# Optimization experiments

Measured on AMD Instinct MI355X. Metric: run time of the kernel, lower is better.

The kernel has to match this reference:

```python
import jax, jax.numpy as jnp
import numpy as np

N_EXPERTS = 8
D_MODEL = 1024
D_FF = 4096
BATCH = 4
SEQ = 4096


def setup_inputs() -> dict:
    key = jax.random.key(0)
    k1, k2, k3, k4 = jax.random.split(key, 4)
    hidden_states = jax.random.normal(k1, (BATCH, SEQ, D_MODEL), dtype=jnp.float32)
    expert_indices = jax.random.randint(k2, (BATCH, SEQ), 0, N_EXPERTS, dtype=jnp.int64)
    # Expert MLP params, scaled like standard init
    W1 = jax.random.normal(k3, (N_EXPERTS, D_MODEL, D_FF), dtype=jnp.float32) / np.sqrt(D_MODEL)
    b1 = jnp.zeros((N_EXPERTS, D_FF), dtype=jnp.float32)
    W2 = jax.random.normal(k4, (N_EXPERTS, D_FF, D_MODEL), dtype=jnp.float32) / np.sqrt(D_FF)
    b2 = jnp.zeros((N_EXPERTS, D_MODEL), dtype=jnp.float32)
    return {"hidden_states": hidden_states, "expert_indices": expert_indices,
            "W1": W1, "b1": b1, "W2": W2, "b2": b2}


def reference(hidden_states, expert_indices, W1, b1, W2, b2):
    B, S, D = hidden_states.shape
    flat = hidden_states.reshape(B * S, D)          # [T, D]
    idx = expert_indices.reshape(-1)                 # [T]
    out = jnp.zeros_like(flat)
    # Fixed small loop over experts (structurally distinct weights).
    # jit-friendly: each expert runs over all tokens, output masked per token.
    for e in range(W1.shape[0]):
        h = jax.nn.gelu(flat @ W1[e] + b1[e])        # [T, F]
        y = h @ W2[e] + b2[e]                        # [T, D]
        out = out + jnp.where((idx == e)[:, None], y, jnp.float32(0.0))
    return out.reshape(B, S, D)
```

## Files before the change

### kernel.cpp

```cpp
#include <hip/hip_runtime.h>

#define T_TOK 16384
#define DMODEL 1024
#define DFF 4096
#define NEXP 8
#define BM 128
#define BN 128
#define BK 32
#define LDA 40
#define LDB 40
#define TPAD (T_TOK + NEXP * BM)

typedef __bf16 bf16x8 __attribute__((ext_vector_type(8)));
typedef float f32x4 __attribute__((ext_vector_type(4)));

#define GLOAD16(gp, lp) __builtin_amdgcn_global_load_lds( \
    (const __attribute__((address_space(1))) void*)(gp), \
    (__attribute__((address_space(3))) void*)(lp), 16, 0, 0)

__device__ __forceinline__ float gelu_f(float x) {
  float u = 0.7978845608028654f * (x + 0.044715f * x * x * x);
  float e = __expf(2.0f * u);
  float th = 1.0f - 2.0f / (e + 1.0f);
  return 0.5f * x * (1.0f + th);
}

__global__ void k_init(int* counts, int* cursors, int* bucket, int n) {
  int i = blockIdx.x * blockDim.x + threadIdx.x;
  if (i < n) bucket[i] = -1;
  if (i < NEXP) { counts[i] = 0; cursors[i] = 0; }
}

__global__ void k_hist(const int* __restrict__ idx, int* counts) {
  int t = blockIdx.x * blockDim.x + threadIdx.x;
  if (t < T_TOK) atomicAdd(&counts[idx[t]], 1);
}

__global__ void k_scan(const int* __restrict__ counts, int* po) {
  if (threadIdx.x == 0 && blockIdx.x == 0) {
    int acc = 0;
    for (int e = 0; e < NEXP; e++) {
      po[e] = acc;
      acc += ((counts[e] + BM - 1) / BM) * BM;
    }
    po[NEXP] = acc;
  }
}

__global__ void k_scatter(const int* __restrict__ idx, const int* __restrict__ po,
                          int* cursors, int* bucket) {
  int t = blockIdx.x * blockDim.x + threadIdx.x;
  if (t < T_TOK) {
    int e = idx[t];
    int p = atomicAdd(&cursors[e], 1);
    bucket[po[e] + p] = t;
  }
}

__global__ __launch_bounds__(256) void k_gather(
    const float* __restrict__ X, const int* __restrict__ bucket,
    __bf16* __restrict__ Xg)
{
  const int r = blockIdx.x;
  const int t = bucket[r];
  const int c = threadIdx.x * 4;
  float4 v = {0.f, 0.f, 0.f, 0.f};
  if (t >= 0) v = *(const float4*)&X[(size_t)t * DMODEL + c];
  union { __bf16 h[4]; uint2 u; } cv;
  cv.h[0] = (__bf16)v.x; cv.h[1] = (__bf16)v.y;
  cv.h[2] = (__bf16)v.z; cv.h[3] = (__bf16)v.w;
  *(uint2*)&Xg[(size_t)r * DMODEL + c] = cv.u;
}

__global__ __launch_bounds__(256) void k_transpose(
    const float* __restrict__ W, __bf16* __restrict__ Wt, int K, int N)
{
  __shared__ float tile[64][65];
  const size_t msz = (size_t)K * N;
  const float* __restrict__ src = W + (size_t)blockIdx.z * msz;
  __bf16* __restrict__ dst = Wt + (size_t)blockIdx.z * msz;
  const int n0 = blockIdx.x * 64, k0 = blockIdx.y * 64;
  const int tc = threadIdx.x & 15, tr = threadIdx.x >> 4;
#pragma unroll
  for (int i = 0; i < 4; i++) {
    float4 v = *(const float4*)&src[(size_t)(k0 + tr + i * 16) * N + n0 + tc * 4];
    tile[tr + i * 16][tc * 4 + 0] = v.x;
    tile[tr + i * 16][tc * 4 + 1] = v.y;
    tile[tr + i * 16][tc * 4 + 2] = v.z;
    tile[tr + i * 16][tc * 4 + 3] = v.w;
  }
  __syncthreads();
#pragma unroll
  for (int i = 0; i < 4; i++) {
    const int n = tr + i * 16;
    union { __bf16 h[4]; uint2 u; } cv;
    cv.h[0] = (__bf16)tile[tc * 4 + 0][n];
    cv.h[1] = (__bf16)tile[tc * 4 + 1][n];
    cv.h[2] = (__bf16)tile[tc * 4 + 2][n];
    cv.h[3] = (__bf16)tile[tc * 4 + 3][n];
    *(uint2*)&dst[(size_t)(n0 + n) * K + k0 + tc * 4] = cv.u;
  }
}

__global__ __launch_bounds__(256, 2) void k_gemm1b(
    const __bf16* __restrict__ Ag, const __bf16* __restrict__ Wt,
    const float* __restrict__ b1, const int* __restrict__ po,
    __bf16* __restrict__ H)
{
  __shared__ __align__(16) __bf16 As[BM * BK];
  __shared__ __align__(16) __bf16 Bs[BN * BK];
  const int tid = threadIdx.x;
  const int row0 = (int)blockIdx.x * BM;
  if (row0 >= po[NEXP]) return;
  const int nb0 = (int)blockIdx.y * BN;

  int e = 0;
#pragma unroll
  for (int k = 1; k < NEXP; k++) e = (row0 >= po[k]) ? k : e;
  const __bf16* __restrict__ B = Wt + (size_t)e * DFF * DMODEL;

  f32x4 acc[4][4];
#pragma unroll
  for (int i = 0; i < 4; i++)
#pragma unroll
    for (int j = 0; j < 4; j++) acc[i][j] = (f32x4)0.0f;

  const int wave = tid >> 6;
  const int lane = tid & 63;
  const int wm = (wave & 1) * 64;
  const int wn = (wave >> 1) * 64;
  const int lm = lane & 15;
  const int lq = lane >> 4;

  const int sr = wave * 32 + (lane >> 2);
  const int skq = lane & 3;
  const __bf16* Aptr = Ag + (size_t)(row0 + sr) * DMODEL + skq * 8;
  const __bf16* Bptr = B + (size_t)(nb0 + sr) * DMODEL + skq * 8;
  __bf16* Al = &As[wave * 1024];
  __bf16* Bl = &Bs[wave * 1024];

  for (int k0 = 0; k0 < DMODEL; k0 += BK) {
    GLOAD16(Aptr + k0, Al);
    GLOAD16(Aptr + k0 + 16 * DMODEL, Al + 512);
    GLOAD16(Bptr + k0, Bl);
    GLOAD16(Bptr + k0 + 16 * DMODEL, Bl + 512);
    __syncthreads();

    bf16x8 af[4], bfr[4];
#pragma unroll
    for (int i = 0; i < 4; i++)
      af[i] = *(const bf16x8*)&As[(wm + i * 16 + lm) * BK + lq * 8];
#pragma unroll
    for (int j = 0; j < 4; j++)
      bfr[j] = *(const bf16x8*)&Bs[(wn + j * 16 + lm) * BK + lq * 8];
#pragma unroll
    for (int i = 0; i < 4; i++)
#pragma unroll
      for (int j = 0; j < 4; j++)
        acc[i][j] = __builtin_amdgcn_mfma_f32_16x16x32_bf16(af[i], bfr[j], acc[i][j], 0, 0, 0);
    __syncthreads();
  }

  const float* __restrict__ b1e = b1 + e * DFF;
#pragma unroll
  for (int j = 0; j < 4; j++) {
    const int col = nb0 + wn + j * 16 + lm;
    const float bias = b1e[col];
#pragma unroll
    for (int i = 0; i < 4; i++) {
#pragma unroll
      for (int r = 0; r < 4; r++) {
        int row = row0 + wm + i * 16 + lq * 4 + r;
        H[(size_t)row * DFF + col] = (__bf16)gelu_f(acc[i][j][r] + bias);
      }
    }
  }
}

__global__ __launch_bounds__(256, 2) void k_gemm2b(
    const __bf16* __restrict__ H, const __bf16* __restrict__ Wt,
    const float* __restrict__ b2, const int* __restrict__ bucket,
    const int* __restrict__ po, float* __restrict__ out)
{
  __shared__ __align__(16) __bf16 As[BM * BK];
  __shared__ __align__(16) __bf16 Bs[BN * BK];
  __shared__ int toks[BM];
  const int tid = threadIdx.x;
  const int row0 = (int)blockIdx.x * BM;
  if (row0 >= po[NEXP]) return;
  const int nb0 = (int)blockIdx.y * BN;

  int e = 0;
#pragma unroll
  for (int k = 1; k < NEXP; k++) e = (row0 >= po[k]) ? k : e;
  const __bf16* __restrict__ B = Wt + (size_t)e * DMODEL * DFF;

  if (tid < BM) toks[tid] = bucket[row0 + tid];

  f32x4 acc[4][4];
#pragma unroll
  for (int i = 0; i < 4; i++)
#pragma unroll
    for (int j = 0; j < 4; j++) acc[i][j] = (f32x4)0.0f;

  const int wave = tid >> 6;
  const int lane = tid & 63;
  const int wm = (wave & 1) * 64;
  const int wn = (wave >> 1) * 64;
  const int lm = lane & 15;
  const int lq = lane >> 4;

  const int sr = wave * 32 + (lane >> 2);
  const int skq = lane & 3;
  const __bf16* Aptr = H + (size_t)(row0 + sr) * DFF + skq * 8;
  const __bf16* Bptr = B + (size_t)(nb0 + sr) * DFF + skq * 8;
  __bf16* Al = &As[wave * 1024];
  __bf16* Bl = &Bs[wave * 1024];

  for (int k0 = 0; k0 < DFF; k0 += BK) {
    GLOAD16(Aptr + k0, Al);
    GLOAD16(Aptr + k0 + 16 * DFF, Al + 512);
    GLOAD16(Bptr + k0, Bl);
    GLOAD16(Bptr + k0 + 16 * DFF, Bl + 512);
    __syncthreads();

    bf16x8 af[4], bfr[4];
#pragma unroll
    for (int i = 0; i < 4; i++)
      af[i] = *(const bf16x8*)&As[(wm + i * 16 + lm) * BK + lq * 8];
#pragma unroll
    for (int j = 0; j < 4; j++)
      bfr[j] = *(const bf16x8*)&Bs[(wn + j * 16 + lm) * BK + lq * 8];
#pragma unroll
    for (int i = 0; i < 4; i++)
#pragma unroll
      for (int j = 0; j < 4; j++)
        acc[i][j] = __builtin_amdgcn_mfma_f32_16x16x32_bf16(af[i], bfr[j], acc[i][j], 0, 0, 0);
    __syncthreads();
  }

  const float* __restrict__ b2e = b2 + e * DMODEL;
#pragma unroll
  for (int j = 0; j < 4; j++) {
    const int col = nb0 + wn + j * 16 + lm;
    const float bias = b2e[col];
#pragma unroll
    for (int i = 0; i < 4; i++) {
#pragma unroll
      for (int r = 0; r < 4; r++) {
        int t = toks[wm + i * 16 + lq * 4 + r];
        if (t >= 0) out[(size_t)t * DMODEL + col] = acc[i][j][r] + bias;
      }
    }
  }
}

__global__ __launch_bounds__(256, 2) void k_gemm1(
    const float* __restrict__ X, const float* __restrict__ W1,
    const float* __restrict__ b1, const int* __restrict__ bucket,
    const int* __restrict__ po, __bf16* __restrict__ H, int base_row)
{
  __shared__ __bf16 As[BM * LDA];
  __shared__ __bf16 Bs[BN * LDB];
  __shared__ int toks[BM];
  const int tid = threadIdx.x;
  const int total = po[NEXP];
  const int row0 = base_row + (int)blockIdx.x * BM;
  if (row0 >= total) return;
  const int nb0 = (int)blockIdx.y * BN;
  int e = 0;
#pragma unroll
  for (int k = 1; k < NEXP; k++) e = (row0 >= po[k]) ? k : e;
  const float* __restrict__ W = W1 + (size_t)e * DMODEL * DFF;
  if (tid < BM) toks[tid] = bucket[row0 + tid];
  __syncthreads();
  f32x4 acc[4][4];
#pragma unroll
  for (int i = 0; i < 4; i++)
#pragma unroll
    for (int j = 0; j < 4; j++) acc[i][j] = (f32x4)0.0f;
  const int wave = tid >> 6, lane = tid & 63;
  const int wm = (wave & 1) * 64, wn = (wave >> 1) * 64;
  const int lm = lane & 15, lq = lane >> 4;
  const int bn = tid & 127, bkh = (tid >> 7) * 16;
  for (int k0 = 0; k0 < DMODEL; k0 += BK) {
#pragma unroll
    for (int i = 0; i < 4; i++) {
      int idx = tid + i * 256;
      int row = idx >> 3, kq = idx & 7;
      int t = toks[row];
      float4 v = {0.f, 0.f, 0.f, 0.f};
      if (t >= 0) v = *(const float4*)(X + (size_t)t * DMODEL + k0 + kq * 4);
      union { __bf16 h[4]; uint2 u; } cv;
      cv.h[0] = (__bf16)v.x; cv.h[1] = (__bf16)v.y;
      cv.h[2] = (__bf16)v.z; cv.h[3] = (__bf16)v.w;
      *(uint2*)&As[row * LDA + kq * 4] = cv.u;
    }
    {
      const float* src = W + (size_t)(k0 + bkh) * DFF + nb0 + bn;
      bf16x8 b0, b1v;
#pragma unroll
      for (int kk = 0; kk < 8; kk++) b0[kk] = (__bf16)src[(size_t)kk * DFF];
#pragma unroll
      for (int kk = 0; kk < 8; kk++) b1v[kk] = (__bf16)src[(size_t)(kk + 8) * DFF];
      *(bf16x8*)&Bs[bn * LDB + bkh] = b0;
      *(bf16x8*)&Bs[bn * LDB + bkh + 8] = b1v;
    }
    __syncthreads();
    bf16x8 af[4], bfr[4];
#pragma unroll
    for (int i = 0; i < 4; i++)
      af[i] = *(const bf16x8*)&As[(wm + i * 16 + lm) * LDA + lq * 8];
#pragma unroll
    for (int j = 0; j < 4; j++)
      bfr[j] = *(const bf16x8*)&Bs[(wn + j * 16 + lm) * LDB + lq * 8];
#pragma unroll
    for (int i = 0; i < 4; i++)
#pragma unroll
      for (int j = 0; j < 4; j++)
        acc[i][j] = __builtin_amdgcn_mfma_f32_16x16x32_bf16(af[i], bfr[j], acc[i][j], 0, 0, 0);
    __syncthreads();
  }
  const float* __restrict__ b1e = b1 + e * DFF;
  const int hbase = (int)blockIdx.x * BM;
#pragma unroll
  for (int j = 0; j < 4; j++) {
    const int col = nb0 + wn + j * 16 + lm;
    const float bias = b1e[col];
#pragma unroll
    for (int i = 0; i < 4; i++)
#pragma unroll
      for (int r = 0; r < 4; r++) {
        int row = hbase + wm + i * 16 + lq * 4 + r;
        H[(size_t)row * DFF + col] = (__bf16)gelu_f(acc[i][j][r] + bias);
      }
  }
}

__global__ __launch_bounds__(256, 2) void k_gemm2(
    const __bf16* __restrict__ H, const float* __restrict__ W2,
    const float* __restrict__ b2, const int* __restrict__ bucket,
    const int* __restrict__ po, float* __restrict__ out, int base_row)
{
  __shared__ __bf16 As[BM * LDA];
  __shared__ __bf16 Bs[BN * LDB];
  __shared__ int toks[BM];
  const int tid = threadIdx.x;
  const int total = po[NEXP];
  const int row0 = base_row + (int)blockIdx.x * BM;
  if (row0 >= total) return;
  const int nb0 = (int)blockIdx.y * BN;
  int e = 0;
#pragma unroll
  for (int k = 1; k < NEXP; k++) e = (row0 >= po[k]) ? k : e;
  const float* __restrict__ W = W2 + (size_t)e * DFF * DMODEL;
  if (tid < BM) toks[tid] = bucket[row0 + tid];
  __syncthreads();
  f32x4 acc[4][4];
#pragma unroll
  for (int i = 0; i < 4; i++)
#pragma unroll
    for (int j = 0; j < 4; j++) acc[i][j] = (f32x4)0.0f;
  const int wave = tid >> 6, lane = tid & 63;
  const int wm = (wave & 1) * 64, wn = (wave >> 1) * 64;
  const int lm = lane & 15, lq = lane >> 4;
  const int bn = tid & 127, bkh = (tid >> 7) * 16;
  const int hbase = (int)blockIdx.x * BM;
  for (int k0 = 0; k0 < DFF; k0 += BK) {
#pragma unroll
    for (int i = 0; i < 2; i++) {
      int idx = tid + i * 256;
      int row = idx >> 2, kq = idx & 3;
      bf16x8 v = *(const bf16x8*)(H + (size_t)(hbase + row) * DFF + k0 + kq * 8);
      *(bf16x8*)&As[row * LDA + kq * 8] = v;
    }
    {
      const float* src = W + (size_t)(k0 + bkh) * DMODEL + nb0 + bn;
      bf16x8 b0, b1v;
#pragma unroll
      for (int kk = 0; kk < 8; kk++) b0[kk] = (__bf16)src[(size_t)kk * DMODEL];
#pragma unroll
      for (int kk = 0; kk < 8; kk++) b1v[kk] = (__bf16)src[(size_t)(kk + 8) * DMODEL];
      *(bf16x8*)&Bs[bn * LDB + bkh] = b0;
      *(bf16x8*)&Bs[bn * LDB + bkh + 8] = b1v;
    }
    __syncthreads();
    bf16x8 af[4], bfr[4];
#pragma unroll
    for (int i = 0; i < 4; i++)
      af[i] = *(const bf16x8*)&As[(wm + i * 16 + lm) * LDA + lq * 8];
#pragma unroll
    for (int j = 0; j < 4; j++)
      bfr[j] = *(const bf16x8*)&Bs[(wn + j * 16 + lm) * LDB + lq * 8];
#pragma unroll
    for (int i = 0; i < 4; i++)
#pragma unroll
      for (int j = 0; j < 4; j++)
        acc[i][j] = __builtin_amdgcn_mfma_f32_16x16x32_bf16(af[i], bfr[j], acc[i][j], 0, 0, 0);
    __syncthreads();
  }
  const float* __restrict__ b2e = b2 + e * DMODEL;
#pragma unroll
  for (int j = 0; j < 4; j++) {
    const int col = nb0 + wn + j * 16 + lm;
    const float bias = b2e[col];
#pragma unroll
    for (int i = 0; i < 4; i++)
#pragma unroll
      for (int r = 0; r < 4; r++) {
        int t = toks[wm + i * 16 + lq * 4 + r];
        if (t >= 0) out[(size_t)t * DMODEL + col] = acc[i][j][r] + bias;
      }
  }
}

__global__ __launch_bounds__(256) void k_fallback(
    const float* __restrict__ X, const int* __restrict__ idx,
    const float* __restrict__ W1, const float* __restrict__ b1,
    const float* __restrict__ W2, const float* __restrict__ b2,
    float* __restrict__ out)
{
  __shared__ float xs[DMODEL];
  __shared__ float hs[DFF];
  const int t = blockIdx.x;
  const int e = idx[t];
  const int tid = threadIdx.x;
  const float* w1 = W1 + (size_t)e * DMODEL * DFF;
  const float* w2 = W2 + (size_t)e * DFF * DMODEL;
  for (int i = tid; i < DMODEL; i += 256) xs[i] = X[(size_t)t * DMODEL + i];
  __syncthreads();
  for (int f = tid; f < DFF; f += 256) {
    float a = 0.f;
    for (int d = 0; d < DMODEL; d++) a += xs[d] * w1[(size_t)d * DFF + f];
    hs[f] = gelu_f(a + b1[e * DFF + f]);
  }
  __syncthreads();
  for (int d = tid; d < DMODEL; d += 256) {
    float a = 0.f;
    for (int f = 0; f < DFF; f++) a += hs[f] * w2[(size_t)f * DMODEL + d];
    out[(size_t)t * DMODEL + d] = a + b2[e * DMODEL + d];
  }
}

extern "C" void kernel_launch(void* const* d_in, const int* in_sizes, int n_in,
                              void* d_out, int out_size, void* d_ws, size_t ws_size,
                              hipStream_t stream) {
  const float* X  = (const float*)d_in[0];
  const int*   EI = (const int*)d_in[1];
  const float* W1 = (const float*)d_in[2];
  const float* b1 = (const float*)d_in[3];
  const float* W2 = (const float*)d_in[4];
  const float* b2 = (const float*)d_in[5];
  float* out = (float*)d_out;

  char* ws = (char*)d_ws;
  int* counts  = (int*)(ws + 0);
  int* cursors = (int*)(ws + 32);
  int* po      = (int*)(ws + 64);
  int* bucket  = (int*)(ws + 512);
  const int Tpad = TPAD;

  const size_t XG_OFF = 70144;
  const size_t XG_SZ  = (size_t)Tpad * DMODEL * 2;
  const size_t WT_OFF = XG_OFF + XG_SZ;
  const size_t WT_SZ  = (size_t)NEXP * DMODEL * DFF * 2;
  const size_t HF_OFF = WT_OFF + WT_SZ;
  const size_t H_SZ   = (size_t)Tpad * DFF * 2;
  const size_t NEED   = HF_OFF + H_SZ;

  if (ws_size >= NEED) {
    __bf16* Xg = (__bf16*)(ws + XG_OFF);
    __bf16* Wt = (__bf16*)(ws + WT_OFF);
    __bf16* H  = (__bf16*)(ws + HF_OFF);

    k_init<<<(Tpad + 255) / 256, 256, 0, stream>>>(counts, cursors, bucket, Tpad);
    k_hist<<<(T_TOK + 255) / 256, 256, 0, stream>>>(EI, counts);
    k_scan<<<1, 64, 0, stream>>>(counts, po);
    k_scatter<<<(T_TOK + 255) / 256, 256, 0, stream>>>(EI, po, cursors, bucket);
    k_gather<<<Tpad, 256, 0, stream>>>(X, bucket, Xg);
    k_transpose<<<dim3(DFF / 64, DMODEL / 64, NEXP), 256, 0, stream>>>(W1, Wt, DMODEL, DFF);
    k_gemm1b<<<dim3(Tpad / BM, DFF / BN), 256, 0, stream>>>(Xg, Wt, b1, po, H);
    k_transpose<<<dim3(DMODEL / 64, DFF / 64, NEXP), 256, 0, stream>>>(W2, Wt, DFF, DMODEL);
    k_gemm2b<<<dim3(Tpad / BM, DMODEL / BN), 256, 0, stream>>>(H, Wt, b2, bucket, po, out);
    return;
  }

  const size_t H_OFF = 512 + (size_t)Tpad * 4;
  __bf16* H = (__bf16*)(ws + H_OFF);
  size_t avail = (ws_size > H_OFF) ? ws_size - H_OFF : 0;
  long long crll = (long long)(avail / ((size_t)DFF * 2));
  int CR = (crll > Tpad) ? Tpad : (int)crll;
  CR -= CR % BM;
  if (CR < BM) {
    k_fallback<<<T_TOK, 256, 0, stream>>>(X, EI, W1, b1, W2, b2, out);
    return;
  }
  k_init<<<(Tpad + 255) / 256, 256, 0, stream>>>(counts, cursors, bucket, Tpad);
  k_hist<<<(T_TOK + 255) / 256, 256, 0, stream>>>(EI, counts);
  k_scan<<<1, 64, 0, stream>>>(counts, po);
  k_scatter<<<(T_TOK + 255) / 256, 256, 0, stream>>>(EI, po, cursors, bucket);
  int nchunks = (Tpad + CR - 1) / CR;
  for (int c = 0; c < nchunks; c++) {
    int base = c * CR;
    int rows = Tpad - base; if (rows > CR) rows = CR;
    int mt = rows / BM;
    k_gemm1<<<dim3(mt, DFF / BN), 256, 0, stream>>>(X, W1, b1, bucket, po, H, base);
    k_gemm2<<<dim3(mt, DMODEL / BN), 256, 0, stream>>>(H, W2, b2, bucket, po, out, base);
  }
}
```

Measured before the change: 1.056 ms.

## Swizzle LDS layout and remap block grid in expert GEMMs

Both expert GEMM kernels now XOR-swizzle the 16-byte chunk position when loading global data into LDS and when reading fragments, so that fragment reads hit fewer LDS bank conflicts. The 2D grid is also flattened into 1D with a grouped mapping: eight consecutive blocks share a column tile and cover eight row tiles, which is meant to improve L2 reuse of weight and activation tiles. The block remapping assumes Tpad/BM is a multiple of 8, and the swizzle has to match exactly between the load and read sides.

```diff
diff --git a/kernel.cpp b/kernel.cpp
--- a/kernel.cpp
+++ b/kernel.cpp
@@ -110,9 +110,13 @@
   __shared__ __align__(16) __bf16 As[BM * BK];
   __shared__ __align__(16) __bf16 Bs[BN * BK];
   const int tid = threadIdx.x;
-  const int row0 = (int)blockIdx.x * BM;
+  const int b = (int)blockIdx.x;
+  const int slot = b >> 3;
+  const int row_t = (b & 7) + ((slot >> 5) << 3);
+  const int col_t = slot & 31;
+  const int row0 = row_t * BM;
   if (row0 >= po[NEXP]) return;
-  const int nb0 = (int)blockIdx.y * BN;
+  const int nb0 = col_t * BN;
 
   int e = 0;
 #pragma unroll
@@ -133,11 +137,13 @@
   const int lq = lane >> 4;
 
   const int sr = wave * 32 + (lane >> 2);
-  const int skq = lane & 3;
-  const __bf16* Aptr = Ag + (size_t)(row0 + sr) * DMODEL + skq * 8;
-  const __bf16* Bptr = B + (size_t)(nb0 + sr) * DMODEL + skq * 8;
+  const int g  = (lane & 3) ^ ((lane >> 3) & 3);
+  const __bf16* Aptr = Ag + (size_t)(row0 + sr) * DMODEL + g * 8;
+  const __bf16* Bptr = B + (size_t)(nb0 + sr) * DMODEL + g * 8;
   __bf16* Al = &As[wave * 1024];
   __bf16* Bl = &Bs[wave * 1024];
+
+  const int sA = (lm >> 1) & 3;
 
   for (int k0 = 0; k0 < DMODEL; k0 += BK) {
     GLOAD16(Aptr + k0, Al);
@@ -149,10 +155,10 @@
     bf16x8 af[4], bfr[4];
 #pragma unroll
     for (int i = 0; i < 4; i++)
-      af[i] = *(const bf16x8*)&As[(wm + i * 16 + lm) * BK + lq * 8];
+      af[i] = *(const bf16x8*)&As[(wm + i * 16 + lm) * BK + (lq ^ sA) * 8];
 #pragma unroll
     for (int j = 0; j < 4; j++)
-      bfr[j] = *(const bf16x8*)&Bs[(wn + j * 16 + lm) * BK + lq * 8];
+      bfr[j] = *(const bf16x8*)&Bs[(wn + j * 16 + lm) * BK + (lq ^ sA) * 8];
 #pragma unroll
     for (int i = 0; i < 4; i++)
 #pragma unroll
@@ -186,9 +192,13 @@
   __shared__ __align__(16) __bf16 Bs[BN * BK];
   __shared__ int toks[BM];
   const int tid = threadIdx.x;
-  const int row0 = (int)blockIdx.x * BM;
+  const int b = (int)blockIdx.x;
+  const int slot = b >> 3;
+  const int row_t = (b & 7) + ((slot >> 3) << 3);
+  const int col_t = slot & 7;
+  const int row0 = row_t * BM;
   if (row0 >= po[NEXP]) return;
-  const int nb0 = (int)blockIdx.y * BN;
+  const int nb0 = col_t * BN;
 
   int e = 0;
 #pragma unroll
@@ -211,11 +221,12 @@
   const int lq = lane >> 4;
 
   const int sr = wave * 32 + (lane >> 2);
-  const int skq = lane & 3;
-  const __bf16* Aptr = H + (size_t)(row0 + sr) * DFF + skq * 8;
-  const __bf16* Bptr = B + (size_t)(nb0 + sr) * DFF + skq * 8;
+  const int g  = (lane & 3) ^ ((lane >> 3) & 3);
+  const __bf16* Aptr = H + (size_t)(row0 + sr) * DFF + g * 8;
+  const __bf16* Bptr = B + (size_t)(nb0 + sr) * DFF + g * 8;
   __bf16* Al = &As[wave * 1024];
   __bf16* Bl = &Bs[wave * 1024];
+  const int sA = (lm >> 1) & 3;
 
   for (int k0 = 0; k0 < DFF; k0 += BK) {
     GLOAD16(Aptr + k0, Al);
@@ -227,10 +238,10 @@
     bf16x8 af[4], bfr[4];
 #pragma unroll
     for (int i = 0; i < 4; i++)
-      af[i] = *(const bf16x8*)&As[(wm + i * 16 + lm) * BK + lq * 8];
+      af[i] = *(const bf16x8*)&As[(wm + i * 16 + lm) * BK + (lq ^ sA) * 8];
 #pragma unroll
     for (int j = 0; j < 4; j++)
-      bfr[j] = *(const bf16x8*)&Bs[(wn + j * 16 + lm) * BK + lq * 8];
+      bfr[j] = *(const bf16x8*)&Bs[(wn + j * 16 + lm) * BK + (lq ^ sA) * 8];
 #pragma unroll
     for (int i = 0; i < 4; i++)
 #pragma unroll
@@ -479,9 +490,9 @@
     k_scatter<<<(T_TOK + 255) / 256, 256, 0, stream>>>(EI, po, cursors, bucket);
     k_gather<<<Tpad, 256, 0, stream>>>(X, bucket, Xg);
     k_transpose<<<dim3(DFF / 64, DMODEL / 64, NEXP), 256, 0, stream>>>(W1, Wt, DMODEL, DFF);
-    k_gemm1b<<<dim3(Tpad / BM, DFF / BN), 256, 0, stream>>>(Xg, Wt, b1, po, H);
+    k_gemm1b<<<(Tpad / BM) * (DFF / BN), 256, 0, stream>>>(Xg, Wt, b1, po, H);
     k_transpose<<<dim3(DMODEL / 64, DFF / 64, NEXP), 256, 0, stream>>>(W2, Wt, DFF, DMODEL);
-    k_gemm2b<<<dim3(Tpad / BM, DMODEL / BN), 256, 0, stream>>>(H, Wt, b2, bucket, po, out);
+    k_gemm2b<<<(Tpad / BM) * (DMODEL / BN), 256, 0, stream>>>(H, Wt, b2, bucket, po, out);
     return;
   }
 
```

Measured after the change: 965.6 us. 8.6% less time.
